# Optimization experiments

Hardware: AMD Instinct MI355X
Metric: run time of the kernel (lower is better)

The kernel has to match this reference:

```python
import jax, jax.numpy as jnp
import numpy as np

N = 100000   # nodes
E = 1600000  # edges (avg degree 16)
DN = 16      # node_attr_dim
DE = 8       # edge_attr_dim
H = 32       # node_emb_dim
L = 7        # num_gnn_layers


def setup_inputs() -> dict:
    key = jax.random.key(0)
    ks = jax.random.split(key, 8)
    s = 0.05
    return {
        "x": jax.random.normal(ks[0], (N, DN), jnp.float32),
        "edge_attr": jax.random.normal(ks[1], (E, DE), jnp.float32),
        "edge_index": jax.random.randint(ks[2], (2, E), 0, N),
        # node_init_mlp: Linear(DN -> H)
        "W_node": jax.random.normal(ks[3], (DN, H), jnp.float32) * s,
        "b_node": jnp.zeros((H,), jnp.float32),
        # per-layer message_mlp: Linear(H+DE -> H)
        "Wm": jax.random.normal(ks[4], (L, H + DE, H), jnp.float32) * s,
        "bm": jnp.zeros((L, H), jnp.float32),
        # per-layer update_mlp: Linear(H -> H) followed by ReLU
        "Wu": jax.random.normal(ks[5], (L, H, H), jnp.float32) * s,
        "bu": jnp.zeros((L, H), jnp.float32),
        # post_mlp: Linear(H -> 1)
        "W_post": jax.random.normal(ks[6], (H, 1), jnp.float32) * s,
        "b_post": jnp.zeros((1,), jnp.float32),
    }


def reference(x, edge_attr, edge_index, W_node, b_node, Wm, bm, Wu, bu, W_post, b_post):
    src = edge_index[0]  # x_j (source)
    dst = edge_index[1]  # aggregation index (target, PyG source_to_target)

    h = x @ W_node + b_node  # node_init_mlp: [N, H]

    def layer(h, params):
        Wm_l, bm_l, Wu_l, bu_l = params
        # message: concat([x_j, edge_attr]) -> Linear (extended_message_in_flag=False)
        msg_in = jnp.concatenate([h[src], edge_attr], axis=-1)  # [E, H+DE]
        msg = msg_in @ Wm_l + bm_l                              # [E, H]
        # aggregate: scatter-max onto target nodes
        aggr = jax.ops.segment_max(msg, dst, num_segments=N)    # [N, H]
        aggr = jnp.where(jnp.isneginf(aggr), 0.0, aggr)         # empty segments -> 0
        # update: ReLU(Linear(aggr)) (update_with_target_flag=False)
        upd = jax.nn.relu(aggr @ Wu_l + bu_l)
        # inter-layer bypass (residual)
        return h + upd, None

    h, _ = jax.lax.scan(layer, h, (Wm, bm, Wu, bu))
    return h @ W_post + b_post  # post_mlp: [N, 1]
```

## Files before the change

### kernel.cpp

```cpp
#include <hip/hip_runtime.h>

#define NN 100000
#define NE 1600000
#define DN 16
#define DE 8
#define H  32
#define NL 7
#define CAP 64

#define SCAN_BT   1024
#define SCAN_NB   ((NN + SCAN_BT - 1) / SCAN_BT)
#define BSUM_T    128


__global__ __launch_bounds__(256) void zero_cnt_kernel(int* __restrict__ cnt) {
    int i = blockIdx.x * blockDim.x + threadIdx.x;
    if (i < NN) cnt[i] = 0;
}

__global__ __launch_bounds__(256) void slot_scatter_kernel(
        const int* __restrict__ dst, int* __restrict__ cnt,
        int* __restrict__ slots) {
    int e = blockIdx.x * blockDim.x + threadIdx.x;
    if (e >= NE) return;
    int d = dst[e];
    int pos = atomicAdd(&cnt[d], 1);
    if (pos < CAP) slots[(long)d * CAP + pos] = e;
}

__global__ __launch_bounds__(256) void hist_kernel(const int* __restrict__ dst,
                                                   int* __restrict__ cnt) {
    int e = blockIdx.x * blockDim.x + threadIdx.x;
    if (e < NE) atomicAdd(&cnt[dst[e]], 1);
}

__global__ __launch_bounds__(SCAN_BT) void scan_partial_kernel(
        const int* __restrict__ cnt, int* __restrict__ bsum, int cap) {
    __shared__ int red[SCAN_BT];
    int t = threadIdx.x;
    int i = blockIdx.x * SCAN_BT + t;
    red[t] = (i < NN) ? min(cnt[i], cap) : 0;
    __syncthreads();
    for (int off = SCAN_BT / 2; off > 0; off >>= 1) {
        if (t < off) red[t] += red[t + off];
        __syncthreads();
    }
    if (t == 0) bsum[blockIdx.x] = red[0];
}

__global__ __launch_bounds__(BSUM_T) void scan_bsum_kernel(
        const int* __restrict__ bsum, int* __restrict__ boff,
        int* __restrict__ rowstart) {
    __shared__ int part[BSUM_T];
    int t = threadIdx.x;
    int v = (t < SCAN_NB) ? bsum[t] : 0;
    part[t] = v;
    __syncthreads();
    for (int off = 1; off < BSUM_T; off <<= 1) {
        int add = (t >= off) ? part[t - off] : 0;
        __syncthreads();
        part[t] += add;
        __syncthreads();
    }
    if (t < SCAN_NB) boff[t] = part[t] - v;
    if (t == BSUM_T - 1) rowstart[NN] = part[t];
}

__global__ __launch_bounds__(SCAN_BT) void scan_final_kernel(
        const int* __restrict__ cnt, const int* __restrict__ boff,
        int* __restrict__ rowstart, int* __restrict__ cursor, int cap) {
    __shared__ int part[SCAN_BT];
    int t = threadIdx.x;
    int i = blockIdx.x * SCAN_BT + t;
    int v = (i < NN) ? min(cnt[i], cap) : 0;
    part[t] = v;
    __syncthreads();
    for (int off = 1; off < SCAN_BT; off <<= 1) {
        int add = (t >= off) ? part[t - off] : 0;
        __syncthreads();
        part[t] += add;
        __syncthreads();
    }
    if (i < NN) {
        int r = boff[blockIdx.x] + part[t] - v;
        rowstart[i] = r;
        cursor[i]   = r;
    }
}

__global__ __launch_bounds__(256) void compact_kernel(
        const int* __restrict__ slots, const int* __restrict__ rowstart,
        const int* __restrict__ src, const float* __restrict__ ea,
        int* __restrict__ es, float* __restrict__ eas) {
    int tid  = blockIdx.x * blockDim.x + threadIdx.x;
    int node = tid >> 4;
    int lane = tid & 15;
    if (node >= NN) return;
    int lo = rowstart[node];
    int deg = rowstart[node + 1] - lo;
    for (int k = lane; k < deg; k += 16) {
        int e = slots[(long)node * CAP + k];
        es[lo + k] = src[e];
        const float4* s4 = (const float4*)(ea + (long)e * DE);
        float4 a = s4[0], b = s4[1];
        float4* d4 = (float4*)(eas + (long)(lo + k) * DE);
        d4[0] = a; d4[1] = b;
    }
}

__global__ __launch_bounds__(256) void scatter_combined_kernel(
        const int* __restrict__ src, const int* __restrict__ dst,
        const float* __restrict__ ea,
        int* __restrict__ cursor,
        int* __restrict__ es, float* __restrict__ eas) {
    int e = blockIdx.x * blockDim.x + threadIdx.x;
    if (e >= NE) return;
    int pos = atomicAdd(&cursor[dst[e]], 1);
    es[pos] = src[e];
    const float4* s4 = (const float4*)(ea + (long)e * DE);
    float4 a = s4[0], b = s4[1];
    float4* d4 = (float4*)(eas + (long)pos * DE);
    d4[0] = a; d4[1] = b;
}

__global__ __launch_bounds__(256) void init_kernel(
        const float* __restrict__ x,
        const float* __restrict__ W_node, const float* __restrict__ b_node,
        const float* __restrict__ Wm0, const float* __restrict__ bm0,
        float* __restrict__ h, float* __restrict__ hm)
{
    int n = blockIdx.x * blockDim.x + threadIdx.x;
    if (n >= NN) return;

    float xin[DN];
    #pragma unroll
    for (int k = 0; k < DN/4; ++k) {
        float4 v = ((const float4*)(x + (long)n*DN))[k];
        xin[4*k+0]=v.x; xin[4*k+1]=v.y; xin[4*k+2]=v.z; xin[4*k+3]=v.w;
    }
    float hv[H];
    #pragma unroll
    for (int j = 0; j < H; ++j) hv[j] = b_node[j];
    #pragma unroll
    for (int k = 0; k < DN; ++k)
        #pragma unroll
        for (int j = 0; j < H; ++j)
            hv[j] = fmaf(xin[k], W_node[k*H+j], hv[j]);

    #pragma unroll
    for (int j = 0; j < H/4; ++j)
        ((float4*)(h + (long)n*H))[j] = make_float4(hv[4*j],hv[4*j+1],hv[4*j+2],hv[4*j+3]);

    float hmv[H];
    #pragma unroll
    for (int j = 0; j < H; ++j) hmv[j] = bm0[j];
    #pragma unroll
    for (int k = 0; k < H; ++k)
        #pragma unroll
        for (int j = 0; j < H; ++j)
            hmv[j] = fmaf(hv[k], Wm0[k*H+j], hmv[j]);

    #pragma unroll
    for (int j = 0; j < H/4; ++j)
        ((float4*)(hm + (long)n*H))[j] = make_float4(hmv[4*j],hmv[4*j+1],hmv[4*j+2],hmv[4*j+3]);
}

#define MSG_FMA(A, B, M0, M1)                                         \
    M0 = fmaf(A.x, w0[0], M0);  M1 = fmaf(A.x, w1[0], M1);            \
    M0 = fmaf(A.y, w0[1], M0);  M1 = fmaf(A.y, w1[1], M1);            \
    M0 = fmaf(A.z, w0[2], M0);  M1 = fmaf(A.z, w1[2], M1);            \
    M0 = fmaf(A.w, w0[3], M0);  M1 = fmaf(A.w, w1[3], M1);            \
    M0 = fmaf(B.x, w0[4], M0);  M1 = fmaf(B.x, w1[4], M1);            \
    M0 = fmaf(B.y, w0[5], M0);  M1 = fmaf(B.y, w1[5], M1);            \
    M0 = fmaf(B.z, w0[6], M0);  M1 = fmaf(B.z, w1[6], M1);            \
    M0 = fmaf(B.w, w0[7], M0);  M1 = fmaf(B.w, w1[7], M1);

__global__ __launch_bounds__(256) void aggr_kernel(
        const int* __restrict__ rowstart, const int* __restrict__ es,
        const float* __restrict__ eas,
        const float* __restrict__ Wm_bot,
        const float* __restrict__ hm,
        float* __restrict__ aggr)
{
    int tid  = blockIdx.x * blockDim.x + threadIdx.x;
    int node = tid >> 4;
    int sub  = tid & 15;
    if (node >= NN) return;

    float w0[DE], w1[DE];
    #pragma unroll
    for (int k = 0; k < DE; ++k) {
        w0[k] = Wm_bot[k*H + sub*2 + 0];
        w1[k] = Wm_bot[k*H + sub*2 + 1];
    }

    float acc0 = -__builtin_inff(), acc1 = -__builtin_inff();

    int lo = rowstart[node], hi = rowstart[node+1];
    int i = lo;

    for (; i + 3 < hi; i += 4) {
        int s0 = es[i], s1 = es[i+1], s2 = es[i+2], s3 = es[i+3];
        float2 hv0 = *(const float2*)(hm + (long)s0*H + sub*2);
        float2 hv1 = *(const float2*)(hm + (long)s1*H + sub*2);
        float2 hv2 = *(const float2*)(hm + (long)s2*H + sub*2);
        float2 hv3 = *(const float2*)(hm + (long)s3*H + sub*2);
        const float4* p0 = (const float4*)(eas + (long)i * DE);
        const float4* p1 = (const float4*)(eas + (long)(i+1) * DE);
        const float4* p2 = (const float4*)(eas + (long)(i+2) * DE);
        const float4* p3 = (const float4*)(eas + (long)(i+3) * DE);
        float4 a0 = p0[0], b0 = p0[1];
        float4 a1 = p1[0], b1 = p1[1];
        float4 a2 = p2[0], b2 = p2[1];
        float4 a3 = p3[0], b3 = p3[1];
        float m00 = hv0.x, m01 = hv0.y;
        float m10 = hv1.x, m11 = hv1.y;
        float m20 = hv2.x, m21 = hv2.y;
        float m30 = hv3.x, m31 = hv3.y;
        MSG_FMA(a0, b0, m00, m01)
        MSG_FMA(a1, b1, m10, m11)
        MSG_FMA(a2, b2, m20, m21)
        MSG_FMA(a3, b3, m30, m31)
        acc0 = fmaxf(acc0, fmaxf(fmaxf(m00, m10), fmaxf(m20, m30)));
        acc1 = fmaxf(acc1, fmaxf(fmaxf(m01, m11), fmaxf(m21, m31)));
    }
    for (; i + 1 < hi; i += 2) {
        int s0 = es[i], s1 = es[i+1];
        float2 hv0 = *(const float2*)(hm + (long)s0*H + sub*2);
        float2 hv1 = *(const float2*)(hm + (long)s1*H + sub*2);
        const float4* p0 = (const float4*)(eas + (long)i * DE);
        const float4* p1 = (const float4*)(eas + (long)(i+1) * DE);
        float4 a0 = p0[0], b0 = p0[1];
        float4 a1 = p1[0], b1 = p1[1];
        float m00 = hv0.x, m01 = hv0.y;
        float m10 = hv1.x, m11 = hv1.y;
        MSG_FMA(a0, b0, m00, m01)
        MSG_FMA(a1, b1, m10, m11)
        acc0 = fmaxf(acc0, fmaxf(m00, m10));
        acc1 = fmaxf(acc1, fmaxf(m01, m11));
    }
    if (i < hi) {
        int s0 = es[i];
        float2 hv0 = *(const float2*)(hm + (long)s0*H + sub*2);
        const float4* p0 = (const float4*)(eas + (long)i * DE);
        float4 a0 = p0[0], b0 = p0[1];
        float m00 = hv0.x, m01 = hv0.y;
        MSG_FMA(a0, b0, m00, m01)
        acc0 = fmaxf(acc0, m00);
        acc1 = fmaxf(acc1, m01);
    }
    if (lo == hi) { acc0 = 0.f; acc1 = 0.f; }
    *(float2*)(aggr + (long)node*H + sub*2) = make_float2(acc0, acc1);
}

__global__ __launch_bounds__(256) void update_kernel(
        const float* __restrict__ Wu, const float* __restrict__ bu,
        const float* __restrict__ Wm_next, const float* __restrict__ bm_next,
        const float* __restrict__ W_post, const float* __restrict__ b_post,
        float* __restrict__ h, float* __restrict__ hm,
        const float* __restrict__ aggr, float* __restrict__ out, int last)
{
    int n = blockIdx.x * blockDim.x + threadIdx.x;
    if (n >= NN) return;

    float av[H];
    #pragma unroll
    for (int j = 0; j < H/4; ++j) {
        float4 v = ((const float4*)(aggr + (long)n*H))[j];
        av[4*j+0]=v.x; av[4*j+1]=v.y; av[4*j+2]=v.z; av[4*j+3]=v.w;
    }

    float uv[H];
    #pragma unroll
    for (int j = 0; j < H; ++j) uv[j] = bu[j];
    #pragma unroll
    for (int k = 0; k < H; ++k)
        #pragma unroll
        for (int j = 0; j < H; ++j)
            uv[j] = fmaf(av[k], Wu[k*H+j], uv[j]);

    float hv[H];
    #pragma unroll
    for (int j = 0; j < H/4; ++j) {
        float4 v = ((const float4*)(h + (long)n*H))[j];
        hv[4*j+0]=v.x; hv[4*j+1]=v.y; hv[4*j+2]=v.z; hv[4*j+3]=v.w;
    }
    #pragma unroll
    for (int j = 0; j < H; ++j) hv[j] += fmaxf(uv[j], 0.f);

    #pragma unroll
    for (int j = 0; j < H/4; ++j)
        ((float4*)(h + (long)n*H))[j] = make_float4(hv[4*j],hv[4*j+1],hv[4*j+2],hv[4*j+3]);

    if (!last) {
        float hmv[H];
        #pragma unroll
        for (int j = 0; j < H; ++j) hmv[j] = bm_next[j];
        #pragma unroll
        for (int k = 0; k < H; ++k)
            #pragma unroll
            for (int j = 0; j < H; ++j)
                hmv[j] = fmaf(hv[k], Wm_next[k*H+j], hmv[j]);
        #pragma unroll
        for (int j = 0; j < H/4; ++j)
            ((float4*)(hm + (long)n*H))[j] = make_float4(hmv[4*j],hmv[4*j+1],hmv[4*j+2],hmv[4*j+3]);
    } else {
        float acc = b_post[0];
        #pragma unroll
        for (int k = 0; k < H; ++k) acc = fmaf(hv[k], W_post[k], acc);
        out[n] = acc;
    }
}

extern "C" void kernel_launch(void* const* d_in, const int* in_sizes, int n_in,
                              void* d_out, int out_size, void* d_ws, size_t ws_size,
                              hipStream_t stream)
{
    const float* x         = (const float*)d_in[0];
    const float* edge_attr = (const float*)d_in[1];
    const int*   edge_index= (const int*)  d_in[2];
    const float* W_node    = (const float*)d_in[3];
    const float* b_node    = (const float*)d_in[4];
    const float* Wm        = (const float*)d_in[5];
    const float* bm        = (const float*)d_in[6];
    const float* Wu        = (const float*)d_in[7];
    const float* bu        = (const float*)d_in[8];
    const float* W_post    = (const float*)d_in[9];
    const float* b_post    = (const float*)d_in[10];
    float* out = (float*)d_out;

    const int* src = edge_index;
    const int* dst = edge_index + NE;

    char* ws = (char*)d_ws;
    size_t off = 0;
    float* h        = (float*)(ws + off); off += (size_t)NN*H*4;
    float* hm       = (float*)(ws + off); off += (size_t)NN*H*4;
    float* aggr     = (float*)(ws + off); off += (size_t)NN*H*4;
    int*   cnt      = (int*)  (ws + off); off += (size_t)NN*4;
    int*   rowstart = (int*)  (ws + off); off += (size_t)(NN+16)*4;
    int*   cursor   = (int*)  (ws + off); off += (size_t)NN*4;
    int*   bsum     = (int*)  (ws + off); off += (size_t)256*4;
    int*   boff     = (int*)  (ws + off); off += (size_t)256*4;
    int*   es       = (int*)  (ws + off); off += (size_t)NE*4;
    float* eas      = (float*)(ws + off); off += (size_t)NE*DE*4;
    size_t slots_off = off;
    int*   slots    = (int*)  (ws + slots_off);
    const int use_slots = (ws_size >= slots_off + (size_t)NN*CAP*4);

    const int nodeBlocks  = (NN + 255) / 256;
    const int edgeBlocks  = (NE + 255) / 256;
    const int aggrBlocks  = (NN*16 + 255) / 256;

    zero_cnt_kernel<<<nodeBlocks, 256, 0, stream>>>(cnt);
    if (use_slots) {
        slot_scatter_kernel<<<edgeBlocks, 256, 0, stream>>>(dst, cnt, slots);
        scan_partial_kernel<<<SCAN_NB, SCAN_BT, 0, stream>>>(cnt, bsum, CAP);
        scan_bsum_kernel<<<1, BSUM_T, 0, stream>>>(bsum, boff, rowstart);
        scan_final_kernel<<<SCAN_NB, SCAN_BT, 0, stream>>>(cnt, boff, rowstart, cursor, CAP);
        compact_kernel<<<aggrBlocks, 256, 0, stream>>>(slots, rowstart, src, edge_attr, es, eas);
    } else {
        hist_kernel<<<edgeBlocks, 256, 0, stream>>>(dst, cnt);
        scan_partial_kernel<<<SCAN_NB, SCAN_BT, 0, stream>>>(cnt, bsum, 0x7FFFFFFF);
        scan_bsum_kernel<<<1, BSUM_T, 0, stream>>>(bsum, boff, rowstart);
        scan_final_kernel<<<SCAN_NB, SCAN_BT, 0, stream>>>(cnt, boff, rowstart, cursor, 0x7FFFFFFF);
        scatter_combined_kernel<<<edgeBlocks, 256, 0, stream>>>(src, dst, edge_attr,
                                                                cursor, es, eas);
    }

    init_kernel<<<nodeBlocks, 256, 0, stream>>>(x, W_node, b_node, Wm, bm, h, hm);

    for (int l = 0; l < NL; ++l) {
        const float* Wm_l   = Wm + (size_t)l*(H+DE)*H;
        const float* Wm_bot = Wm_l + (size_t)H*H;
        const float* Wu_l   = Wu + (size_t)l*H*H;
        const float* bu_l   = bu + (size_t)l*H;
        int last = (l == NL-1);
        const float* Wm_next = last ? nullptr : Wm + (size_t)(l+1)*(H+DE)*H;
        const float* bm_next = last ? nullptr : bm + (size_t)(l+1)*H;

        aggr_kernel<<<aggrBlocks, 256, 0, stream>>>(rowstart, es, eas, Wm_bot, hm, aggr);
        update_kernel<<<nodeBlocks, 256, 0, stream>>>(Wu_l, bu_l, Wm_next, bm_next,
                                                      W_post, b_post, h, hm, aggr, out, last);
    }
}
```

Baseline: 974.9 us.

## Replace atomic slot-based CSR build with two-level bucket counting sort

Builds the destination-sorted edge list with a coarse counting sort over 128-node buckets, using per-block shared-memory histograms, a global scan and a scatter. A per-bucket fine sort in shared memory then produces row starts and the permuted source and edge-attribute arrays. This replaces the per-edge global atomics and the padded per-node slot array, aiming to cut global atomic contention and scattered memory traffic during preprocessing. It adds more kernel launches and an intermediate int2 edge buffer, and it drops the CAP=64 truncation, so nodes with high in-degree are no longer cut off.

```diff
diff --git a/kernel.cpp b/kernel.cpp
--- a/kernel.cpp
+++ b/kernel.cpp
@@ -6,121 +6,134 @@
 #define DE 8
 #define H  32
 #define NL 7
-#define CAP 64
-
-#define SCAN_BT   1024
-#define SCAN_NB   ((NN + SCAN_BT - 1) / SCAN_BT)
-#define BSUM_T    128
-
-
-__global__ __launch_bounds__(256) void zero_cnt_kernel(int* __restrict__ cnt) {
-    int i = blockIdx.x * blockDim.x + threadIdx.x;
-    if (i < NN) cnt[i] = 0;
-}
-
-__global__ __launch_bounds__(256) void slot_scatter_kernel(
-        const int* __restrict__ dst, int* __restrict__ cnt,
-        int* __restrict__ slots) {
-    int e = blockIdx.x * blockDim.x + threadIdx.x;
-    if (e >= NE) return;
-    int d = dst[e];
-    int pos = atomicAdd(&cnt[d], 1);
-    if (pos < CAP) slots[(long)d * CAP + pos] = e;
-}
-
-__global__ __launch_bounds__(256) void hist_kernel(const int* __restrict__ dst,
-                                                   int* __restrict__ cnt) {
-    int e = blockIdx.x * blockDim.x + threadIdx.x;
-    if (e < NE) atomicAdd(&cnt[dst[e]], 1);
-}
-
-__global__ __launch_bounds__(SCAN_BT) void scan_partial_kernel(
-        const int* __restrict__ cnt, int* __restrict__ bsum, int cap) {
-    __shared__ int red[SCAN_BT];
+
+#define NBKT  ((NN + 127) >> 7)
+#define CBLK  256
+#define EPB   ((NE + CBLK - 1) / CBLK)
+#define GCN   (NBKT * CBLK)
+#define G_BT  1024
+#define G_NB  ((GCN + G_BT - 1) / G_BT)
+#define G_BSUM_T 256
+
+
+__global__ __launch_bounds__(256) void coarse_hist_kernel(
+        const int* __restrict__ dst, int* __restrict__ gcountsT) {
+    __shared__ int hist[NBKT];
+    int blk = blockIdx.x, t = threadIdx.x;
+    for (int i = t; i < NBKT; i += 256) hist[i] = 0;
+    __syncthreads();
+    int lo = blk * EPB, hi = min(lo + EPB, NE);
+    for (int i = lo + t; i < hi; i += 256)
+        atomicAdd(&hist[dst[i] >> 7], 1);
+    __syncthreads();
+    for (int i = t; i < NBKT; i += 256)
+        gcountsT[i * CBLK + blk] = hist[i];
+}
+
+__global__ __launch_bounds__(G_BT) void scanG_partial_kernel(
+        const int* __restrict__ in, int* __restrict__ bsum) {
+    __shared__ int red[G_BT];
     int t = threadIdx.x;
-    int i = blockIdx.x * SCAN_BT + t;
-    red[t] = (i < NN) ? min(cnt[i], cap) : 0;
-    __syncthreads();
-    for (int off = SCAN_BT / 2; off > 0; off >>= 1) {
+    int i = blockIdx.x * G_BT + t;
+    red[t] = (i < GCN) ? in[i] : 0;
+    __syncthreads();
+    for (int off = G_BT / 2; off > 0; off >>= 1) {
         if (t < off) red[t] += red[t + off];
         __syncthreads();
     }
     if (t == 0) bsum[blockIdx.x] = red[0];
 }
 
-__global__ __launch_bounds__(BSUM_T) void scan_bsum_kernel(
-        const int* __restrict__ bsum, int* __restrict__ boff,
-        int* __restrict__ rowstart) {
-    __shared__ int part[BSUM_T];
+__global__ __launch_bounds__(G_BSUM_T) void scanG_bsum_kernel(
+        const int* __restrict__ bsum, int* __restrict__ boff) {
+    __shared__ int part[G_BSUM_T];
     int t = threadIdx.x;
-    int v = (t < SCAN_NB) ? bsum[t] : 0;
+    int v = (t < G_NB) ? bsum[t] : 0;
     part[t] = v;
     __syncthreads();
-    for (int off = 1; off < BSUM_T; off <<= 1) {
+    for (int off = 1; off < G_BSUM_T; off <<= 1) {
         int add = (t >= off) ? part[t - off] : 0;
         __syncthreads();
         part[t] += add;
         __syncthreads();
     }
-    if (t < SCAN_NB) boff[t] = part[t] - v;
-    if (t == BSUM_T - 1) rowstart[NN] = part[t];
-}
-
-__global__ __launch_bounds__(SCAN_BT) void scan_final_kernel(
-        const int* __restrict__ cnt, const int* __restrict__ boff,
-        int* __restrict__ rowstart, int* __restrict__ cursor, int cap) {
-    __shared__ int part[SCAN_BT];
+    if (t < G_NB) boff[t] = part[t] - v;
+}
+
+__global__ __launch_bounds__(G_BT) void scanG_final_kernel(
+        const int* __restrict__ in, const int* __restrict__ boff,
+        int* __restrict__ out) {
+    __shared__ int part[G_BT];
     int t = threadIdx.x;
-    int i = blockIdx.x * SCAN_BT + t;
-    int v = (i < NN) ? min(cnt[i], cap) : 0;
+    int i = blockIdx.x * G_BT + t;
+    int v = (i < GCN) ? in[i] : 0;
     part[t] = v;
     __syncthreads();
-    for (int off = 1; off < SCAN_BT; off <<= 1) {
+    for (int off = 1; off < G_BT; off <<= 1) {
         int add = (t >= off) ? part[t - off] : 0;
         __syncthreads();
         part[t] += add;
         __syncthreads();
     }
-    if (i < NN) {
-        int r = boff[blockIdx.x] + part[t] - v;
-        rowstart[i] = r;
-        cursor[i]   = r;
-    }
-}
-
-__global__ __launch_bounds__(256) void compact_kernel(
-        const int* __restrict__ slots, const int* __restrict__ rowstart,
+    if (i < GCN) out[i] = boff[blockIdx.x] + part[t] - v;
+}
+
+__global__ __launch_bounds__(256) void coarse_scatter_kernel(
+        const int* __restrict__ dst, const int* __restrict__ gbaseT,
+        int2* __restrict__ ebkt) {
+    __shared__ int base[NBKT];
+    int blk = blockIdx.x, t = threadIdx.x;
+    for (int i = t; i < NBKT; i += 256)
+        base[i] = gbaseT[i * CBLK + blk];
+    __syncthreads();
+    int lo = blk * EPB, hi = min(lo + EPB, NE);
+    for (int i = lo + t; i < hi; i += 256) {
+        int d = dst[i];
+        int pos = atomicAdd(&base[d >> 7], 1);
+        ebkt[pos] = make_int2(i, d);
+    }
+}
+
+__global__ __launch_bounds__(256) void fine_sort_kernel(
+        const int2* __restrict__ ebkt, const int* __restrict__ gbaseT,
         const int* __restrict__ src, const float* __restrict__ ea,
-        int* __restrict__ es, float* __restrict__ eas) {
-    int tid  = blockIdx.x * blockDim.x + threadIdx.x;
-    int node = tid >> 4;
-    int lane = tid & 15;
-    if (node >= NN) return;
-    int lo = rowstart[node];
-    int deg = rowstart[node + 1] - lo;
-    for (int k = lane; k < deg; k += 16) {
-        int e = slots[(long)node * CAP + k];
-        es[lo + k] = src[e];
+        int* __restrict__ rowstart, int* __restrict__ es, float* __restrict__ eas) {
+    __shared__ int s_hist[128], s_incl[128], s_cur[128];
+    int b = blockIdx.x, t = threadIdx.x;
+    int segstart = gbaseT[b * CBLK];
+    int segend   = (b == NBKT - 1) ? NE : gbaseT[(b + 1) * CBLK];
+
+    if (t < 128) { s_hist[t] = 0; s_cur[t] = 0; }
+    __syncthreads();
+    for (int i = segstart + t; i < segend; i += 256)
+        atomicAdd(&s_hist[ebkt[i].y & 127], 1);
+    __syncthreads();
+    if (t < 128) s_incl[t] = s_hist[t];
+    __syncthreads();
+    for (int off = 1; off < 128; off <<= 1) {
+        int add = (t < 128 && t >= off) ? s_incl[t - off] : 0;
+        __syncthreads();
+        if (t < 128) s_incl[t] += add;
+        __syncthreads();
+    }
+    if (t < 128) {
+        int node = b * 128 + t;
+        if (node < NN) rowstart[node] = segstart + s_incl[t] - s_hist[t];
+    }
+    if (b == NBKT - 1 && t == 0) rowstart[NN] = NE;
+    __syncthreads();
+    for (int i = segstart + t; i < segend; i += 256) {
+        int2 ed = ebkt[i];
+        int j = ed.y & 127;
+        int lp = atomicAdd(&s_cur[j], 1);
+        int pos = segstart + (s_incl[j] - s_hist[j]) + lp;
+        int e = ed.x;
+        es[pos] = src[e];
         const float4* s4 = (const float4*)(ea + (long)e * DE);
-        float4 a = s4[0], b = s4[1];
-        float4* d4 = (float4*)(eas + (long)(lo + k) * DE);
-        d4[0] = a; d4[1] = b;
-    }
-}
-
-__global__ __launch_bounds__(256) void scatter_combined_kernel(
-        const int* __restrict__ src, const int* __restrict__ dst,
-        const float* __restrict__ ea,
-        int* __restrict__ cursor,
-        int* __restrict__ es, float* __restrict__ eas) {
-    int e = blockIdx.x * blockDim.x + threadIdx.x;
-    if (e >= NE) return;
-    int pos = atomicAdd(&cursor[dst[e]], 1);
-    es[pos] = src[e];
-    const float4* s4 = (const float4*)(ea + (long)e * DE);
-    float4 a = s4[0], b = s4[1];
-    float4* d4 = (float4*)(eas + (long)pos * DE);
-    d4[0] = a; d4[1] = b;
+        float4 a = s4[0], bb = s4[1];
+        float4* d4 = (float4*)(eas + (long)pos * DE);
+        d4[0] = a; d4[1] = bb;
+    }
 }
 
 __global__ __launch_bounds__(256) void init_kernel(
@@ -337,36 +350,25 @@
     float* h        = (float*)(ws + off); off += (size_t)NN*H*4;
     float* hm       = (float*)(ws + off); off += (size_t)NN*H*4;
     float* aggr     = (float*)(ws + off); off += (size_t)NN*H*4;
-    int*   cnt      = (int*)  (ws + off); off += (size_t)NN*4;
     int*   rowstart = (int*)  (ws + off); off += (size_t)(NN+16)*4;
-    int*   cursor   = (int*)  (ws + off); off += (size_t)NN*4;
-    int*   bsum     = (int*)  (ws + off); off += (size_t)256*4;
-    int*   boff     = (int*)  (ws + off); off += (size_t)256*4;
     int*   es       = (int*)  (ws + off); off += (size_t)NE*4;
     float* eas      = (float*)(ws + off); off += (size_t)NE*DE*4;
-    size_t slots_off = off;
-    int*   slots    = (int*)  (ws + slots_off);
-    const int use_slots = (ws_size >= slots_off + (size_t)NN*CAP*4);
-
-    const int nodeBlocks  = (NN + 255) / 256;
-    const int edgeBlocks  = (NE + 255) / 256;
-    const int aggrBlocks  = (NN*16 + 255) / 256;
-
-    zero_cnt_kernel<<<nodeBlocks, 256, 0, stream>>>(cnt);
-    if (use_slots) {
-        slot_scatter_kernel<<<edgeBlocks, 256, 0, stream>>>(dst, cnt, slots);
-        scan_partial_kernel<<<SCAN_NB, SCAN_BT, 0, stream>>>(cnt, bsum, CAP);
-        scan_bsum_kernel<<<1, BSUM_T, 0, stream>>>(bsum, boff, rowstart);
-        scan_final_kernel<<<SCAN_NB, SCAN_BT, 0, stream>>>(cnt, boff, rowstart, cursor, CAP);
-        compact_kernel<<<aggrBlocks, 256, 0, stream>>>(slots, rowstart, src, edge_attr, es, eas);
-    } else {
-        hist_kernel<<<edgeBlocks, 256, 0, stream>>>(dst, cnt);
-        scan_partial_kernel<<<SCAN_NB, SCAN_BT, 0, stream>>>(cnt, bsum, 0x7FFFFFFF);
-        scan_bsum_kernel<<<1, BSUM_T, 0, stream>>>(bsum, boff, rowstart);
-        scan_final_kernel<<<SCAN_NB, SCAN_BT, 0, stream>>>(cnt, boff, rowstart, cursor, 0x7FFFFFFF);
-        scatter_combined_kernel<<<edgeBlocks, 256, 0, stream>>>(src, dst, edge_attr,
-                                                                cursor, es, eas);
-    }
+    int2*  ebkt     = (int2*) (ws + off); off += (size_t)NE*8;
+    int*   gcountsT = (int*)  (ws + off); off += (size_t)GCN*4;
+    int*   gbaseT   = (int*)  (ws + off); off += (size_t)GCN*4;
+    int*   bsum2    = (int*)  (ws + off); off += (size_t)G_BT*4;
+    int*   boff2    = (int*)  (ws + off); off += (size_t)G_BT*4;
+
+    const int nodeBlocks = (NN + 255) / 256;
+    const int aggrBlocks = (NN*16 + 255) / 256;
+
+    coarse_hist_kernel   <<<CBLK, 256, 0, stream>>>(dst, gcountsT);
+    scanG_partial_kernel <<<G_NB, G_BT, 0, stream>>>(gcountsT, bsum2);
+    scanG_bsum_kernel    <<<1, G_BSUM_T, 0, stream>>>(bsum2, boff2);
+    scanG_final_kernel   <<<G_NB, G_BT, 0, stream>>>(gcountsT, boff2, gbaseT);
+    coarse_scatter_kernel<<<CBLK, 256, 0, stream>>>(dst, gbaseT, ebkt);
+    fine_sort_kernel     <<<NBKT, 256, 0, stream>>>(ebkt, gbaseT, src, edge_attr,
+                                                    rowstart, es, eas);
 
     init_kernel<<<nodeBlocks, 256, 0, stream>>>(x, W_node, b_node, Wm, bm, h, hm);
 
```

Measured after the change: 885.1 us. -9.2%, faster.
